# Kernel tuning notes

Measured on AMD Instinct MI355X. Metric: run time of the kernel, lower is better.

Reference implementation:

```python
import jax, jax.numpy as jnp
import numpy as np


def setup_inputs() -> dict:
    key = jax.random.key(0)
    k1, k2, k3 = jax.random.split(key, 3)
    b, c, h, w = 4, 124, 64, 64
    x = jax.random.normal(k1, (b, c, h, w), dtype=jnp.float32)
    # 1x1 conv, no bias -> channel-mixing matrix [c_out, c_in]
    Wb = jax.random.normal(k2, (c, c), dtype=jnp.float32) * (1.0 / np.sqrt(c))
    gamma = jax.random.normal(k3, (1,), dtype=jnp.float32) * 0.1
    return {"x": x, "Wb": Wb, "gamma": gamma}


def reference(x, Wb, gamma):
    b, c, h, w = x.shape
    n = h * w
    xf = x.reshape(b, c, n)                      # [b, c, n]
    # NOTE: original code applies convB for B, C, and D (convC/convD unused)
    Bf = jnp.einsum('oc,bcn->bon', Wb, xf)       # [b, c, n]
    # S = softmax(B^T C, dim=last) -> [b, n, n]
    scores = jnp.einsum('bcm,bcn->bmn', Bf, Bf)
    S = jax.nn.softmax(scores, axis=2)
    # E = D @ S^T -> E[b,c,m] = sum_n D[b,c,n] * S[b,m,n]
    E = jnp.einsum('bcn,bmn->bcm', Bf, S).reshape(b, c, h, w)
    return gamma[0] * E + x
```

## Files before the change

### kernel.cpp

```cpp
#include <hip/hip_runtime.h>

typedef short short8 __attribute__((ext_vector_type(8)));
typedef short short4v __attribute__((ext_vector_type(4)));
typedef float floatx4 __attribute__((ext_vector_type(4)));

#define BB 4
#define CC 124
#define CP 128
#define NN 4096
#define NGRP 256
#define NSPLIT 4
#define KSPLIT (NN / NSPLIT)
#define TN 64
#define NCHUNK (KSPLIT / TN)

static __device__ __forceinline__ unsigned short f2bf(float f) {
    unsigned int u = __float_as_uint(f);
    u += 0x7fffu + ((u >> 16) & 1u);
    return (unsigned short)(u >> 16);
}
static __device__ __forceinline__ float bf2f(unsigned short u) {
    return __uint_as_float(((unsigned int)u) << 16);
}

static __device__ __forceinline__ void gl16(const unsigned short* g, unsigned short* l) {
    __builtin_amdgcn_global_load_lds(
        (const __attribute__((address_space(1))) unsigned int*)g,
        (__attribute__((address_space(3))) unsigned int*)l, 16, 0, 0);
}

__global__ __launch_bounds__(256) void bf_proj_kernel(const float* __restrict__ x,
                                                      const float* __restrict__ Wb,
                                                      unsigned short* __restrict__ kfrag,
                                                      unsigned short* __restrict__ vfrag,
                                                      float* __restrict__ m2) {
    __shared__ float xs[CC][68];
    __shared__ float wsh[CP][CC];
    __shared__ float msh[16][64];
    const int tid = threadIdx.x;
    const int b = blockIdx.y;
    const int n0 = blockIdx.x * 64;
    const float* xb = x + (size_t)b * CC * NN + n0;
    for (int i = tid; i < CC * 64; i += 256) {
        int c = i >> 6, n = i & 63;
        xs[c][n] = xb[(size_t)c * NN + n];
    }
    for (int i = tid; i < CC * CC; i += 256) wsh[i / CC][i % CC] = Wb[i];
    for (int i = tid; i < 4 * CC; i += 256) wsh[CC + i / CC][i % CC] = 0.0f;
    __syncthreads();
    const int og = tid >> 4;
    const int n4 = (tid & 15) * 4;
    const int o0 = og * 8;
    float acc[8][4];
#pragma unroll
    for (int k = 0; k < 8; ++k)
#pragma unroll
        for (int j = 0; j < 4; ++j) acc[k][j] = 0.f;
    for (int c = 0; c < CC; ++c) {
        floatx4 xv = *(const floatx4*)&xs[c][n4];
#pragma unroll
        for (int k = 0; k < 8; ++k) {
            float wv = wsh[o0 + k][c];
            acc[k][0] += wv * xv[0];
            acc[k][1] += wv * xv[1];
            acc[k][2] += wv * xv[2];
            acc[k][3] += wv * xv[3];
        }
    }
    float sq[4] = {0.f, 0.f, 0.f, 0.f};
#pragma unroll
    for (int k = 0; k < 8; ++k)
#pragma unroll
        for (int j = 0; j < 4; ++j) sq[j] += acc[k][j] * acc[k][j];
#pragma unroll
    for (int j = 0; j < 4; ++j) msh[og][n4 + j] = sq[j];
    const int g = (n0 >> 4) + ((tid >> 2) & 3);
    const int colk = n4 & 15;
    const int tK = o0 >> 5;
    const int qK = (o0 >> 3) & 3;
#pragma unroll
    for (int j = 0; j < 4; ++j) {
        short8 kv;
#pragma unroll
        for (int k = 0; k < 8; ++k) kv[k] = (short)f2bf(acc[k][j]);
        *(short8*)&kfrag[(((size_t)(b * NGRP + g) * 4 + tK) * 64 + qK * 16 + colk + j) * 8] = kv;
    }
    const int s8v = o0 >> 4;
    const int qv = tid & 3;
    const int colv0 = (og & 1) * 8;
#pragma unroll
    for (int k = 0; k < 8; ++k) {
        short4v vv;
#pragma unroll
        for (int j = 0; j < 4; ++j) vv[j] = (short)f2bf(acc[k][j]);
        *(short4v*)&vfrag[(((size_t)(b * NGRP + g) * 8 + s8v) * 64 + qv * 16 + colv0 + k) * 4] = vv;
    }
    __syncthreads();
    if (tid < 64) {
        float s = 0.f;
#pragma unroll
        for (int og2 = 0; og2 < 16; ++og2) s += msh[og2][tid];
        m2[(size_t)b * NN + n0 + tid] = s * 1.44269504088896340736f;
    }
}

__global__ __launch_bounds__(256, 2) void attn_kernel(const unsigned short* __restrict__ kfrag,
                                                      const unsigned short* __restrict__ vfrag,
                                                      const float* __restrict__ m2,
                                                      unsigned short* __restrict__ opart,
                                                      float* __restrict__ ml) {
    __shared__ unsigned short kbuf[2][16 * 64 * 8];
    __shared__ unsigned short vbuf[2][32 * 64 * 4];
    const int id = blockIdx.x;
    const int ghi = id & 7;
    const int r_ = id >> 3;
    const int mtile = r_ & 31;
    const int glo = r_ >> 5;
    const int grp = ghi * 2 + glo;
    const int b = grp & 3;
    const int split = grp >> 2;
    const int w = threadIdx.x >> 6;
    const int lane = threadIdx.x & 63;
    const int col = lane & 15;
    const int m0 = mtile * 128 + w * 32;
    const int g0 = split * (KSPLIT / 16);
    const floatx4 fzero = {0.f, 0.f, 0.f, 0.f};
    const float L2E = 1.44269504088896340736f;

    short8 qf[2][4];
#pragma unroll
    for (int ms = 0; ms < 2; ++ms) {
        const int gq = (m0 >> 4) + ms;
#pragma unroll
        for (int t = 0; t < 4; ++t)
            qf[ms][t] = *(const short8*)&kfrag[(((size_t)(b * NGRP + gq) * 4 + t) * 64 + lane) * 8];
    }
    float mreg[2];
    mreg[0] = m2[(size_t)b * NN + m0 + col];
    mreg[1] = m2[(size_t)b * NN + m0 + 16 + col];

    floatx4 oacc[2][8];
#pragma unroll
    for (int ms = 0; ms < 2; ++ms)
#pragma unroll
        for (int s8 = 0; s8 < 8; ++s8) oacc[ms][s8] = fzero;
    float lsum[2] = {0.f, 0.f};

    auto stage = [&](int ch, int sel) {
        const size_t gg = (size_t)(b * NGRP + g0 + ch * 4 + w);
        const unsigned short* kg = kfrag + gg * 4 * 64 * 8;
        unsigned short* kl = &kbuf[sel][w * 4 * 64 * 8];
#pragma unroll
        for (int t = 0; t < 4; ++t)
            gl16(kg + (size_t)(t * 64 + lane) * 8, kl + t * 64 * 8);
        const unsigned short* vg = vfrag + gg * 8 * 64 * 4;
        unsigned short* vl = &vbuf[sel][w * 8 * 64 * 4];
#pragma unroll
        for (int p = 0; p < 4; ++p)
            gl16(vg + (size_t)(p * 512) + lane * 8, vl + p * 512);
    };

    stage(0, 0);
#pragma unroll 2
    for (int ch = 0; ch < NCHUNK; ++ch) {
        const int sel = ch & 1;
        __syncthreads();
        if (ch + 1 < NCHUNK) stage(ch + 1, sel ^ 1);
        floatx4 st[2][4];
#pragma unroll
        for (int ms = 0; ms < 2; ++ms)
#pragma unroll
            for (int u = 0; u < 4; ++u) st[ms][u] = fzero;
#pragma unroll
        for (int t = 0; t < 4; ++t) {
#pragma unroll
            for (int u = 0; u < 4; ++u) {
                short8 kf = *(const short8*)&kbuf[sel][((u * 4 + t) * 64 + lane) * 8];
                st[0][u] = __builtin_amdgcn_mfma_f32_16x16x32_bf16(kf, qf[0][t], st[0][u], 0, 0, 0);
                st[1][u] = __builtin_amdgcn_mfma_f32_16x16x32_bf16(kf, qf[1][t], st[1][u], 0, 0, 0);
            }
        }
        short4v af[2][4];
#pragma unroll
        for (int ms = 0; ms < 2; ++ms) {
#pragma unroll
            for (int u = 0; u < 4; ++u) {
                float ps = 0.f;
#pragma unroll
                for (int r = 0; r < 4; ++r) {
                    float p = exp2f(__builtin_fmaf(st[ms][u][r], L2E, -mreg[ms]));
                    af[ms][u][r] = (short)f2bf(p);
                    ps += p;
                }
                lsum[ms] += ps;
            }
        }
#pragma unroll
        for (int u = 0; u < 4; ++u) {
#pragma unroll
            for (int s8 = 0; s8 < 8; ++s8) {
                short4v vf = *(const short4v*)&vbuf[sel][((u * 8 + s8) * 64 + lane) * 4];
                oacc[0][s8] = __builtin_amdgcn_mfma_f32_16x16x16bf16_1k(af[0][u], vf, oacc[0][s8], 0, 0, 0);
                oacc[1][s8] = __builtin_amdgcn_mfma_f32_16x16x16bf16_1k(af[1][u], vf, oacc[1][s8], 0, 0, 0);
            }
        }
    }
    const int quad = lane >> 4;
    unsigned short* ob = opart + (size_t)(split * BB + b) * NN * CP;
#pragma unroll
    for (int ms = 0; ms < 2; ++ms)
#pragma unroll
        for (int s8 = 0; s8 < 8; ++s8)
#pragma unroll
            for (int r = 0; r < 4; ++r)
                ob[(size_t)(m0 + ms * 16 + quad * 4 + r) * CP + s8 * 16 + col] = f2bf(oacc[ms][s8][r]);
#pragma unroll
    for (int ms = 0; ms < 2; ++ms) {
        float v = lsum[ms];
        v += __shfl_xor(v, 16);
        v += __shfl_xor(v, 32);
        if (lane < 16)
            ml[(size_t)(split * BB + b) * NN + m0 + ms * 16 + lane] = v;
    }
}

__global__ __launch_bounds__(256) void combine_kernel(const unsigned short* __restrict__ opart,
                                                      const float* __restrict__ ml,
                                                      const float* __restrict__ x,
                                                      const float* __restrict__ gamma,
                                                      float* __restrict__ out) {
    __shared__ float es[32 * 133];
    __shared__ float Lsh[32];
    const int t = threadIdx.x;
    const int b = blockIdx.y;
    const int m0 = blockIdx.x * 32;
    if (t < 32) {
        float L = 0.f;
#pragma unroll
        for (int s = 0; s < NSPLIT; ++s) L += ml[(size_t)(s * BB + b) * NN + m0 + t];
        Lsh[t] = gamma[0] / L;
    }
    const int tc = t & 31, tm = t >> 5;
    float acc[4][4];
#pragma unroll
    for (int i = 0; i < 4; ++i)
#pragma unroll
        for (int j = 0; j < 4; ++j) acc[i][j] = 0.f;
    for (int s = 0; s < NSPLIT; ++s) {
        const unsigned short* obp = opart + ((size_t)(s * BB + b) * NN + m0 + tm * 4) * CP + tc * 4;
#pragma unroll
        for (int i = 0; i < 4; ++i) {
            short4v v = *(const short4v*)(obp + (size_t)i * CP);
            acc[i][0] += bf2f((unsigned short)v[0]);
            acc[i][1] += bf2f((unsigned short)v[1]);
            acc[i][2] += bf2f((unsigned short)v[2]);
            acc[i][3] += bf2f((unsigned short)v[3]);
        }
    }
#pragma unroll
    for (int i = 0; i < 4; ++i)
#pragma unroll
        for (int j = 0; j < 4; ++j) es[(tm * 4 + i) * 133 + tc * 4 + j] = acc[i][j];
    __syncthreads();
    const int wave = t >> 6, lane = t & 63;
    const int half = lane >> 5, lm = lane & 31;
#pragma unroll
    for (int p = 0; p < 16; ++p) {
        int c = p * 8 + wave * 2 + half;
        if (c < CC) {
            size_t base = ((size_t)b * CC + c) * NN + m0 + lm;
            out[base] = es[lm * 133 + c] * Lsh[lm] + x[base];
        }
    }
}

extern "C" void kernel_launch(void* const* d_in, const int* in_sizes, int n_in,
                              void* d_out, int out_size, void* d_ws, size_t ws_size,
                              hipStream_t stream) {
    const float* x = (const float*)d_in[0];
    const float* Wb = (const float*)d_in[1];
    const float* gamma = (const float*)d_in[2];
    float* out = (float*)d_out;

    const size_t kfrag_b = (size_t)BB * NGRP * 4 * 64 * 8 * sizeof(unsigned short);
    const size_t vfrag_b = (size_t)BB * NGRP * 8 * 64 * 4 * sizeof(unsigned short);
    const size_t m2_b = (size_t)BB * NN * sizeof(float);
    const size_t ml_b = (size_t)NSPLIT * BB * NN * sizeof(float);
    const size_t opart_b = (size_t)NSPLIT * BB * NN * CP * sizeof(unsigned short);
    if (ws_size < kfrag_b + vfrag_b + m2_b + ml_b + opart_b) return;

    char* w = (char*)d_ws;
    unsigned short* kfrag = (unsigned short*)w;
    unsigned short* vfrag = (unsigned short*)(w + kfrag_b);
    float* m2 = (float*)(w + kfrag_b + vfrag_b);
    float* ml = (float*)(w + kfrag_b + vfrag_b + m2_b);
    unsigned short* opart = (unsigned short*)(w + kfrag_b + vfrag_b + m2_b + ml_b);

    bf_proj_kernel<<<dim3(NN / 64, BB), 256, 0, stream>>>(x, Wb, kfrag, vfrag, m2);
    attn_kernel<<<dim3(512), 256, 0, stream>>>(kfrag, vfrag, m2, opart, ml);
    combine_kernel<<<dim3(NN / 32, BB), 256, 0, stream>>>(opart, ml, x, gamma, out);
}
```

Measured before the change: 134.9 us.

## Double key splits, fold softmax row-sum into padded V channel, shrink tiles

Raises the key-dimension split count from 4 to 8 and halves the key chunk per iteration, launching 1024 attention blocks with an occupancy hint of 4. The softmax denominator is now computed by the MFMA itself: padding channel 124 of V is set to 1.0, so the per-lane lsum accumulation and the separate ml buffer go away. The projection kernel switches to 32-column tiles with bf16 weights in shared memory, and rounding is replaced by a cheaper round-half-up with packed perm conversion. Staging is split so two waves load K and two load V. Risks include more partial outputs to combine, a bf16-rounded denominator, and higher register pressure under the raised occupancy target.

```diff
diff --git a/kernel.cpp b/kernel.cpp
--- a/kernel.cpp
+++ b/kernel.cpp
@@ -9,19 +9,23 @@
 #define CP 128
 #define NN 4096
 #define NGRP 256
-#define NSPLIT 4
+#define NSPLIT 8
 #define KSPLIT (NN / NSPLIT)
-#define TN 64
+#define TN 32
 #define NCHUNK (KSPLIT / TN)
 
-static __device__ __forceinline__ unsigned short f2bf(float f) {
-    unsigned int u = __float_as_uint(f);
-    u += 0x7fffu + ((u >> 16) & 1u);
-    return (unsigned short)(u >> 16);
+static __device__ __forceinline__ unsigned short f2bf_fast(float f) {
+    return (unsigned short)((__float_as_uint(f) + 0x8000u) >> 16);
 }
 static __device__ __forceinline__ float bf2f(unsigned short u) {
     return __uint_as_float(((unsigned int)u) << 16);
 }
+static __device__ __forceinline__ unsigned int pkbf(float a, float b) {
+    unsigned int ua = __float_as_uint(a) + 0x8000u;
+    unsigned int ub = __float_as_uint(b) + 0x8000u;
+    return __builtin_amdgcn_perm(ub, ua, 0x07060302u);
+}
+union PK2 { short4v s; unsigned int u[2]; };
 
 static __device__ __forceinline__ void gl16(const unsigned short* g, unsigned short* l) {
     __builtin_amdgcn_global_load_lds(
@@ -34,96 +38,103 @@
                                                       unsigned short* __restrict__ kfrag,
                                                       unsigned short* __restrict__ vfrag,
                                                       float* __restrict__ m2) {
-    __shared__ float xs[CC][68];
-    __shared__ float wsh[CP][CC];
-    __shared__ float msh[16][64];
+    __shared__ __align__(16) float xs[CC][36];
+    __shared__ __align__(16) unsigned short wt[CC][CP];
+    __shared__ float msh[32][32];
     const int tid = threadIdx.x;
     const int b = blockIdx.y;
-    const int n0 = blockIdx.x * 64;
+    const int n0 = blockIdx.x * 32;
     const float* xb = x + (size_t)b * CC * NN + n0;
-    for (int i = tid; i < CC * 64; i += 256) {
-        int c = i >> 6, n = i & 63;
-        xs[c][n] = xb[(size_t)c * NN + n];
-    }
-    for (int i = tid; i < CC * CC; i += 256) wsh[i / CC][i % CC] = Wb[i];
-    for (int i = tid; i < 4 * CC; i += 256) wsh[CC + i / CC][i % CC] = 0.0f;
+    for (int i = tid; i < CC * 8; i += 256) {
+        int c = i >> 3, nq = i & 7;
+        *(floatx4*)&xs[c][nq * 4] = *(const floatx4*)(xb + (size_t)c * NN + nq * 4);
+    }
+    for (int i = tid; i < CC * CP; i += 256) {
+        int c = i >> 7, o = i & 127;
+        wt[c][o] = (o < CC) ? f2bf_fast(Wb[o * CC + c]) : (unsigned short)0;
+    }
     __syncthreads();
-    const int og = tid >> 4;
-    const int n4 = (tid & 15) * 4;
-    const int o0 = og * 8;
-    float acc[8][4];
-#pragma unroll
-    for (int k = 0; k < 8; ++k)
+    const int og = tid >> 3;
+    const int nidx = tid & 7;
+    const int o0 = og * 4;
+    float acc[4][4];
+#pragma unroll
+    for (int k = 0; k < 4; ++k)
 #pragma unroll
         for (int j = 0; j < 4; ++j) acc[k][j] = 0.f;
     for (int c = 0; c < CC; ++c) {
-        floatx4 xv = *(const floatx4*)&xs[c][n4];
-#pragma unroll
-        for (int k = 0; k < 8; ++k) {
-            float wv = wsh[o0 + k][c];
-            acc[k][0] += wv * xv[0];
-            acc[k][1] += wv * xv[1];
-            acc[k][2] += wv * xv[2];
-            acc[k][3] += wv * xv[3];
+        floatx4 xv = *(const floatx4*)&xs[c][nidx * 4];
+        short4v wv = *(const short4v*)&wt[c][o0];
+#pragma unroll
+        for (int k = 0; k < 4; ++k) {
+            float wf = bf2f((unsigned short)wv[k]);
+            acc[k][0] += wf * xv[0];
+            acc[k][1] += wf * xv[1];
+            acc[k][2] += wf * xv[2];
+            acc[k][3] += wf * xv[3];
         }
     }
     float sq[4] = {0.f, 0.f, 0.f, 0.f};
 #pragma unroll
-    for (int k = 0; k < 8; ++k)
+    for (int k = 0; k < 4; ++k)
 #pragma unroll
         for (int j = 0; j < 4; ++j) sq[j] += acc[k][j] * acc[k][j];
-#pragma unroll
-    for (int j = 0; j < 4; ++j) msh[og][n4 + j] = sq[j];
-    const int g = (n0 >> 4) + ((tid >> 2) & 3);
-    const int colk = n4 & 15;
+    const int g = (n0 >> 4) + (nidx >> 2);
     const int tK = o0 >> 5;
     const int qK = (o0 >> 3) & 3;
+    const int half = o0 & 7;
 #pragma unroll
     for (int j = 0; j < 4; ++j) {
-        short8 kv;
-#pragma unroll
-        for (int k = 0; k < 8; ++k) kv[k] = (short)f2bf(acc[k][j]);
-        *(short8*)&kfrag[(((size_t)(b * NGRP + g) * 4 + tK) * 64 + qK * 16 + colk + j) * 8] = kv;
-    }
-    const int s8v = o0 >> 4;
-    const int qv = tid & 3;
-    const int colv0 = (og & 1) * 8;
-#pragma unroll
-    for (int k = 0; k < 8; ++k) {
-        short4v vv;
-#pragma unroll
-        for (int j = 0; j < 4; ++j) vv[j] = (short)f2bf(acc[k][j]);
-        *(short4v*)&vfrag[(((size_t)(b * NGRP + g) * 8 + s8v) * 64 + qv * 16 + colv0 + k) * 4] = vv;
-    }
+        PK2 kv;
+        kv.u[0] = pkbf(acc[0][j], acc[1][j]);
+        kv.u[1] = pkbf(acc[2][j], acc[3][j]);
+        size_t unit = ((size_t)(b * NGRP + g) * 4 + tK) * 64 + qK * 16 + ((nidx & 3) * 4 + j);
+        *(short4v*)&kfrag[unit * 8 + half] = kv.s;
+    }
+#pragma unroll
+    for (int k = 0; k < 4; ++k) {
+        int c = o0 + k;
+        PK2 vv;
+        if (c == 124) {
+            vv.u[0] = 0x3f803f80u;
+            vv.u[1] = 0x3f803f80u;
+        } else {
+            vv.u[0] = pkbf(acc[k][0], acc[k][1]);
+            vv.u[1] = pkbf(acc[k][2], acc[k][3]);
+        }
+        size_t unit = ((size_t)(b * NGRP + g) * 8 + (c >> 4)) * 64 + (nidx & 3) * 16 + (c & 15);
+        *(short4v*)&vfrag[unit * 4] = vv.s;
+    }
+#pragma unroll
+    for (int j = 0; j < 4; ++j) msh[og][nidx * 4 + j] = sq[j];
     __syncthreads();
-    if (tid < 64) {
+    if (tid < 32) {
         float s = 0.f;
 #pragma unroll
-        for (int og2 = 0; og2 < 16; ++og2) s += msh[og2][tid];
+        for (int og2 = 0; og2 < 32; ++og2) s += msh[og2][tid];
         m2[(size_t)b * NN + n0 + tid] = s * 1.44269504088896340736f;
     }
 }
 
-__global__ __launch_bounds__(256, 2) void attn_kernel(const unsigned short* __restrict__ kfrag,
+__global__ __launch_bounds__(256, 4) void attn_kernel(const unsigned short* __restrict__ kfrag,
                                                       const unsigned short* __restrict__ vfrag,
                                                       const float* __restrict__ m2,
-                                                      unsigned short* __restrict__ opart,
-                                                      float* __restrict__ ml) {
-    __shared__ unsigned short kbuf[2][16 * 64 * 8];
-    __shared__ unsigned short vbuf[2][32 * 64 * 4];
+                                                      unsigned short* __restrict__ opart) {
+    __shared__ __align__(16) unsigned short kbuf[2][8 * 512];
+    __shared__ __align__(16) unsigned short vbuf[2][8 * 512];
     const int id = blockIdx.x;
     const int ghi = id & 7;
     const int r_ = id >> 3;
     const int mtile = r_ & 31;
     const int glo = r_ >> 5;
-    const int grp = ghi * 2 + glo;
+    const int grp = ghi * 4 + glo;
     const int b = grp & 3;
     const int split = grp >> 2;
     const int w = threadIdx.x >> 6;
     const int lane = threadIdx.x & 63;
     const int col = lane & 15;
     const int m0 = mtile * 128 + w * 32;
-    const int g0 = split * (KSPLIT / 16);
+    const int gsplit = split * (KSPLIT / 16);
     const floatx4 fzero = {0.f, 0.f, 0.f, 0.f};
     const float L2E = 1.44269504088896340736f;
 
@@ -144,20 +155,26 @@
     for (int ms = 0; ms < 2; ++ms)
 #pragma unroll
         for (int s8 = 0; s8 < 8; ++s8) oacc[ms][s8] = fzero;
-    float lsum[2] = {0.f, 0.f};
 
     auto stage = [&](int ch, int sel) {
-        const size_t gg = (size_t)(b * NGRP + g0 + ch * 4 + w);
-        const unsigned short* kg = kfrag + gg * 4 * 64 * 8;
-        unsigned short* kl = &kbuf[sel][w * 4 * 64 * 8];
-#pragma unroll
-        for (int t = 0; t < 4; ++t)
-            gl16(kg + (size_t)(t * 64 + lane) * 8, kl + t * 64 * 8);
-        const unsigned short* vg = vfrag + gg * 8 * 64 * 4;
-        unsigned short* vl = &vbuf[sel][w * 8 * 64 * 4];
-#pragma unroll
-        for (int p = 0; p < 4; ++p)
-            gl16(vg + (size_t)(p * 512) + lane * 8, vl + p * 512);
+        const int gbase = gsplit + ch * 2;
+        if (w < 2) {
+#pragma unroll
+            for (int i = 0; i < 4; ++i) {
+                int p = w * 4 + i;
+                const unsigned short* src =
+                    kfrag + (size_t)(b * NGRP + gbase + (p >> 2)) * 2048 + (p & 3) * 512 + lane * 8;
+                gl16(src, &kbuf[sel][p * 512]);
+            }
+        } else {
+#pragma unroll
+            for (int i = 0; i < 4; ++i) {
+                int q = (w - 2) * 4 + i;
+                const unsigned short* src =
+                    vfrag + (size_t)(b * NGRP + gbase + (q >> 2)) * 2048 + (q & 3) * 512 + lane * 8;
+                gl16(src, &vbuf[sel][q * 512]);
+            }
+        }
     };
 
     stage(0, 0);
@@ -166,37 +183,37 @@
         const int sel = ch & 1;
         __syncthreads();
         if (ch + 1 < NCHUNK) stage(ch + 1, sel ^ 1);
-        floatx4 st[2][4];
+        floatx4 st[2][2];
 #pragma unroll
         for (int ms = 0; ms < 2; ++ms)
 #pragma unroll
-            for (int u = 0; u < 4; ++u) st[ms][u] = fzero;
+            for (int u = 0; u < 2; ++u) st[ms][u] = fzero;
 #pragma unroll
         for (int t = 0; t < 4; ++t) {
 #pragma unroll
-            for (int u = 0; u < 4; ++u) {
+            for (int u = 0; u < 2; ++u) {
                 short8 kf = *(const short8*)&kbuf[sel][((u * 4 + t) * 64 + lane) * 8];
                 st[0][u] = __builtin_amdgcn_mfma_f32_16x16x32_bf16(kf, qf[0][t], st[0][u], 0, 0, 0);
                 st[1][u] = __builtin_amdgcn_mfma_f32_16x16x32_bf16(kf, qf[1][t], st[1][u], 0, 0, 0);
             }
         }
-        short4v af[2][4];
+        short4v af[2][2];
 #pragma unroll
         for (int ms = 0; ms < 2; ++ms) {
 #pragma unroll
-            for (int u = 0; u < 4; ++u) {
-                float ps = 0.f;
-#pragma unroll
-                for (int r = 0; r < 4; ++r) {
-                    float p = exp2f(__builtin_fmaf(st[ms][u][r], L2E, -mreg[ms]));
-                    af[ms][u][r] = (short)f2bf(p);
-                    ps += p;
-                }
-                lsum[ms] += ps;
-            }
-        }
-#pragma unroll
-        for (int u = 0; u < 4; ++u) {
+            for (int u = 0; u < 2; ++u) {
+                float p0 = exp2f(__builtin_fmaf(st[ms][u][0], L2E, -mreg[ms]));
+                float p1 = exp2f(__builtin_fmaf(st[ms][u][1], L2E, -mreg[ms]));
+                float p2 = exp2f(__builtin_fmaf(st[ms][u][2], L2E, -mreg[ms]));
+                float p3 = exp2f(__builtin_fmaf(st[ms][u][3], L2E, -mreg[ms]));
+                PK2 pk;
+                pk.u[0] = pkbf(p0, p1);
+                pk.u[1] = pkbf(p2, p3);
+                af[ms][u] = pk.s;
+            }
+        }
+#pragma unroll
+        for (int u = 0; u < 2; ++u) {
 #pragma unroll
             for (int s8 = 0; s8 < 8; ++s8) {
                 short4v vf = *(const short4v*)&vbuf[sel][((u * 8 + s8) * 64 + lane) * 4];
@@ -213,19 +230,10 @@
         for (int s8 = 0; s8 < 8; ++s8)
 #pragma unroll
             for (int r = 0; r < 4; ++r)
-                ob[(size_t)(m0 + ms * 16 + quad * 4 + r) * CP + s8 * 16 + col] = f2bf(oacc[ms][s8][r]);
-#pragma unroll
-    for (int ms = 0; ms < 2; ++ms) {
-        float v = lsum[ms];
-        v += __shfl_xor(v, 16);
-        v += __shfl_xor(v, 32);
-        if (lane < 16)
-            ml[(size_t)(split * BB + b) * NN + m0 + ms * 16 + lane] = v;
-    }
+                ob[(size_t)(m0 + ms * 16 + quad * 4 + r) * CP + s8 * 16 + col] = f2bf_fast(oacc[ms][s8][r]);
 }
 
 __global__ __launch_bounds__(256) void combine_kernel(const unsigned short* __restrict__ opart,
-                                                      const float* __restrict__ ml,
                                                       const float* __restrict__ x,
                                                       const float* __restrict__ gamma,
                                                       float* __restrict__ out) {
@@ -237,7 +245,8 @@
     if (t < 32) {
         float L = 0.f;
 #pragma unroll
-        for (int s = 0; s < NSPLIT; ++s) L += ml[(size_t)(s * BB + b) * NN + m0 + t];
+        for (int s = 0; s < NSPLIT; ++s)
+            L += bf2f(opart[((size_t)(s * BB + b) * NN + m0 + t) * CP + 124]);
         Lsh[t] = gamma[0] / L;
     }
     const int tc = t & 31, tm = t >> 5;
@@ -285,18 +294,16 @@
     const size_t kfrag_b = (size_t)BB * NGRP * 4 * 64 * 8 * sizeof(unsigned short);
     const size_t vfrag_b = (size_t)BB * NGRP * 8 * 64 * 4 * sizeof(unsigned short);
     const size_t m2_b = (size_t)BB * NN * sizeof(float);
-    const size_t ml_b = (size_t)NSPLIT * BB * NN * sizeof(float);
     const size_t opart_b = (size_t)NSPLIT * BB * NN * CP * sizeof(unsigned short);
-    if (ws_size < kfrag_b + vfrag_b + m2_b + ml_b + opart_b) return;
+    if (ws_size < kfrag_b + vfrag_b + m2_b + opart_b) return;
 
     char* w = (char*)d_ws;
     unsigned short* kfrag = (unsigned short*)w;
     unsigned short* vfrag = (unsigned short*)(w + kfrag_b);
     float* m2 = (float*)(w + kfrag_b + vfrag_b);
-    float* ml = (float*)(w + kfrag_b + vfrag_b + m2_b);
-    unsigned short* opart = (unsigned short*)(w + kfrag_b + vfrag_b + m2_b + ml_b);
-
-    bf_proj_kernel<<<dim3(NN / 64, BB), 256, 0, stream>>>(x, Wb, kfrag, vfrag, m2);
-    attn_kernel<<<dim3(512), 256, 0, stream>>>(kfrag, vfrag, m2, opart, ml);
-    combine_kernel<<<dim3(NN / 32, BB), 256, 0, stream>>>(opart, ml, x, gamma, out);
-}
+    unsigned short* opart = (unsigned short*)(w + kfrag_b + vfrag_b + m2_b);
+
+    bf_proj_kernel<<<dim3(NN / 32, BB), 256, 0, stream>>>(x, Wb, kfrag, vfrag, m2);
+    attn_kernel<<<dim3(1024), 256, 0, stream>>>(kfrag, vfrag, m2, opart);
+    combine_kernel<<<dim3(NN / 32, BB), 256, 0, stream>>>(opart, x, gamma, out);
+}
```

Result: slower. 165.7 us (+22.8%).
